# Kernel tuning notes

Hardware: AMD Instinct MI355X
Metric: run time of the kernel (lower is better)

The kernel has to match this reference:

```python
import jax, jax.numpy as jnp
import numpy as np
from jax import lax

# --- config (matches init_kwargs) ---
H = 1024          # hidden_size
I = 704           # moe_intermediate_size (per expert)
E = 32            # n_routed_experts
G = 8             # n_group
TOPK_GROUP = 3    # topk_group
K = 6             # num_experts_per_tok
N_SHARED = 2      # n_shared_experts -> shared intermediate = N_SHARED * I
SCALE = 1.0       # routed_scaling_factor
T = 2048          # number of tokens
CAP = 2 * (T * K) // E


def setup_inputs() -> dict:
    key = jax.random.key(0)
    ks = jax.random.split(key, 8)
    s = 0.02  # initializer_range
    Is = N_SHARED * I
    return {
        "x": jax.random.normal(ks[0], (T, H), jnp.float32),
        "gate_w": s * jax.random.normal(ks[1], (E, H), jnp.float32),   # router
        "w_gate": s * jax.random.normal(ks[2], (E, H, I), jnp.float32),
        "w_up":   s * jax.random.normal(ks[3], (E, H, I), jnp.float32),
        "w_down": s * jax.random.normal(ks[4], (E, I, H), jnp.float32),
        "sw_gate": s * jax.random.normal(ks[5], (H, Is), jnp.float32),
        "sw_up":   s * jax.random.normal(ks[6], (H, Is), jnp.float32),
        "sw_down": s * jax.random.normal(ks[7], (Is, H), jnp.float32),
    }


def _moe_forward(x, gate_w, w_gate, w_up, w_down, sw_gate, sw_up, sw_down):
    # ---- router: softmax scores + group-limited top-k (topk_method='gready') ----
    logits = x @ gate_w.T                                  # [T, E]
    scores = jax.nn.softmax(logits, axis=-1)               # [T, E]
    group_scores = scores.reshape(T, G, E // G).max(-1)    # [T, G]
    _, gidx = lax.top_k(group_scores, TOPK_GROUP)          # [T, topk_group]
    gmask = jnp.zeros((T, G), scores.dtype).at[jnp.arange(T)[:, None], gidx].set(1.0)
    emask = jnp.repeat(gmask, E // G, axis=1)              # [T, E]
    masked_scores = jnp.where(emask > 0, scores, 0.0)
    topk_w, topk_idx = lax.top_k(masked_scores, K)         # [T, K]
    # norm_topk_prob=False -> weights are raw softmax scores * routed_scaling_factor
    topk_w = topk_w * SCALE

    # ---- dispatch: sort assignments by expert, scatter into [E, CAP, H] buffers ----
    flat_e = topk_idx.reshape(-1)                          # [T*K]
    order = jnp.argsort(flat_e)
    se = flat_e[order]                                     # sorted expert ids
    tok = order // K                                       # source token of each slot
    counts = jax.ops.segment_sum(jnp.ones_like(flat_e), flat_e, num_segments=E)
    starts = jnp.cumsum(counts) - counts
    pos = jnp.arange(T * K) - starts[se]                   # position within expert
    valid = pos < CAP
    pos_w = jnp.where(valid, pos, CAP)                     # overflow slot CAP (sliced off)
    xbuf = jnp.zeros((E, CAP + 1, H), x.dtype).at[se, pos_w].set(x[tok])
    xb = xbuf[:, :CAP]                                     # [E, CAP, H]

    # ---- grouped expert MLPs: silu(x Wg) * (x Wu) @ Wd ----
    g = jnp.einsum("ech,ehi->eci", xb, w_gate)
    u = jnp.einsum("ech,ehi->eci", xb, w_up)
    yb = jnp.einsum("eci,eih->ech", jax.nn.silu(g) * u, w_down)  # [E, CAP, H]

    # ---- combine: gather back and weighted-scatter to tokens ----
    y_flat = yb[se, jnp.minimum(pos, CAP - 1)] * valid[:, None].astype(x.dtype)
    wts = topk_w.reshape(-1)[order]                        # [T*K]
    routed = jnp.zeros((T, H), x.dtype).at[tok].add(y_flat * wts[:, None])

    # ---- shared experts MLP (intermediate = n_shared * moe_inter) ----
    sg = jax.nn.silu(x @ sw_gate) * (x @ sw_up)
    shared = sg @ sw_down

    return routed + shared                                 # [T, H]


def reference(x, gate_w, w_gate, w_up, w_down, sw_gate, sw_up, sw_down):
    return _moe_forward(x, gate_w, w_gate, w_up, w_down, sw_gate, sw_up, sw_down)
```

## Files before the change

### kernel.cpp

```cpp
#include <hip/hip_runtime.h>
#include <hip/hip_bf16.h>

#define H 1024
#define I_DIM 704
#define E 32
#define TOPK_GROUP 3
#define K_TOP 6
#define T_TOK 2048
#define CAP 768
#define IS_DIM 1408
#define NCHUNK 192

typedef __attribute__((ext_vector_type(8))) short short8v;
typedef __attribute__((ext_vector_type(4))) float f32x4;

__device__ __forceinline__ unsigned short f2bfbits(float f) {
  unsigned u = __float_as_uint(f);
  unsigned r = (u + 0x7fffu + ((u >> 16) & 1u)) >> 16;
  return (unsigned short)r;
}
__device__ __forceinline__ unsigned packbf2(float lo, float hi) {
  return (unsigned)f2bfbits(lo) | ((unsigned)f2bfbits(hi) << 16);
}
__device__ __forceinline__ void gload_lds16(const short* g, short* l) {
  __builtin_amdgcn_global_load_lds(
      (const __attribute__((address_space(1))) unsigned int*)g,
      (__attribute__((address_space(3))) unsigned int*)l, 16, 0, 0);
}

__global__ void cast_x_kernel(const float* __restrict__ x, short* __restrict__ xb) {
  size_t i = ((size_t)blockIdx.x * 256 + threadIdx.x) * 4;
  float4 v = *(const float4*)(x + i);
  short4 s;
  s.x = (short)f2bfbits(v.x); s.y = (short)f2bfbits(v.y);
  s.z = (short)f2bfbits(v.z); s.w = (short)f2bfbits(v.w);
  *(short4*)(xb + i) = s;
}

__global__ __launch_bounds__(256) void transpose_cast_kernel(
    const float* __restrict__ in, short* __restrict__ outp,
    int C, int N, long long in_stride, long long out_stride) {
  int e = blockIdx.z;
  const float* src = in + (long long)e * in_stride;
  short* dst = outp + (long long)e * out_stride;
  int n0 = blockIdx.x * 64, c0 = blockIdx.y * 64;
  __shared__ unsigned ldsb[64][34];
  int t = threadIdx.x;
  int n4 = t & 15;
  int kp = t >> 4;
  #pragma unroll
  for (int p = 0; p < 2; ++p) {
    int c = c0 + p * 32 + 2 * kp;
    const float* s0 = src + (long long)c * N + n0 + 4 * n4;
    float4 a = *(const float4*)s0;
    float4 b = *(const float4*)(s0 + N);
    int cc = p * 16 + kp;
    ldsb[4 * n4 + 0][cc] = packbf2(a.x, b.x);
    ldsb[4 * n4 + 1][cc] = packbf2(a.y, b.y);
    ldsb[4 * n4 + 2][cc] = packbf2(a.z, b.z);
    ldsb[4 * n4 + 3][cc] = packbf2(a.w, b.w);
  }
  __syncthreads();
  int ch = t & 7;
  int nr = t >> 3;
  #pragma unroll
  for (int p = 0; p < 2; ++p) {
    int n = p * 32 + nr;
    uint4 v;
    v.x = ldsb[n][4 * ch + 0]; v.y = ldsb[n][4 * ch + 1];
    v.z = ldsb[n][4 * ch + 2]; v.w = ldsb[n][4 * ch + 3];
    *(uint4*)(dst + (size_t)(n0 + n) * C + c0 + 8 * ch) = v;
  }
}

__global__ __launch_bounds__(64) void gating_kernel(const float* __restrict__ x,
                                                    const float* __restrict__ gw,
                                                    int* __restrict__ tidx,
                                                    float* __restrict__ tw) {
  int t = blockIdx.x;
  int lane = threadIdx.x;
  int e = lane & 31, half = lane >> 5;
  const float4* xr4 = (const float4*)(x + (size_t)t * H + half * 512);
  const float4* wr4 = (const float4*)(gw + (size_t)e * H + half * 512);
  double acc = 0.0;
  #pragma unroll 4
  for (int j = 0; j < 128; ++j) {
    float4 a = xr4[j], b = wr4[j];
    acc += (double)a.x * b.x + (double)a.y * b.y + (double)a.z * b.z + (double)a.w * b.w;
  }
  acc += __shfl_down(acc, 32);
  double lg = acc;
  double m = lg;
  #pragma unroll
  for (int off = 16; off >= 1; off >>= 1) {
    double o = __shfl_xor(m, off);
    if (o > m) m = o;
  }
  double p = exp(lg - m);
  double sum = p;
  #pragma unroll
  for (int off = 16; off >= 1; off >>= 1) sum += __shfl_xor(sum, off);
  p /= sum;
  double gmax = p;
  { double o = __shfl_xor(gmax, 1); if (o > gmax) gmax = o;
    o = __shfl_xor(gmax, 2); if (o > gmax) gmax = o; }
  bool gsel = false;
  double gv = gmax;
  #pragma unroll
  for (int it = 0; it < TOPK_GROUP; ++it) {
    double v = gv; int gi = e >> 2;
    #pragma unroll
    for (int off = 16; off >= 1; off >>= 1) {
      double ov = __shfl_xor(v, off);
      int oi = __shfl_xor(gi, off);
      if (ov > v || (ov == v && oi < gi)) { v = ov; gi = oi; }
    }
    if ((e >> 2) == gi) { gsel = true; gv = -1e300; }
  }
  double mp = gsel ? p : 0.0;
  #pragma unroll
  for (int it = 0; it < K_TOP; ++it) {
    double v = mp; int ei = e;
    #pragma unroll
    for (int off = 16; off >= 1; off >>= 1) {
      double ov = __shfl_xor(v, off);
      int oi = __shfl_xor(ei, off);
      if (ov > v || (ov == v && oi < ei)) { v = ov; ei = oi; }
    }
    if (lane == 0) { tidx[t * K_TOP + it] = ei; tw[t * K_TOP + it] = (float)v; }
    if (e == ei) mp = -2.0;
  }
}

__global__ __launch_bounds__(64) void hist_kernel(const int* __restrict__ tidx,
                                                  int* __restrict__ chunk_hist) {
  __shared__ int h[E];
  int c = blockIdx.x, lane = threadIdx.x;
  if (lane < E) h[lane] = 0;
  __syncthreads();
  int te = tidx[c * 64 + lane];
  atomicAdd(&h[te], 1);
  __syncthreads();
  if (lane < E) chunk_hist[c * E + lane] = h[lane];
}

__global__ __launch_bounds__(1024) void scan_kernel(const int* __restrict__ chunk_hist,
                                                    int* __restrict__ chunk_base,
                                                    int* __restrict__ cnt) {
  __shared__ int h[NCHUNK * E];
  int t = threadIdx.x;
  for (int i = t; i < NCHUNK * E; i += 1024) h[i] = chunk_hist[i];
  __syncthreads();
  if (t < E) {
    int run = 0;
    for (int c = 0; c < NCHUNK; ++c) {
      int v = h[c * E + t];
      h[c * E + t] = run;
      run += v;
    }
    cnt[t] = run < CAP ? run : CAP;
  }
  __syncthreads();
  for (int i = t; i < NCHUNK * E; i += 1024) chunk_base[i] = h[i];
}

__global__ __launch_bounds__(64) void place_kernel(const int* __restrict__ tidx,
                                                   const float* __restrict__ tw,
                                                   const int* __restrict__ chunk_base,
                                                   int* __restrict__ token_list,
                                                   float* __restrict__ slot_w) {
  int c = blockIdx.x, lane = threadIdx.x;
  int idx = c * 64 + lane;
  int te = tidx[idx];
  unsigned long long mymask = 0;
  #pragma unroll
  for (int e = 0; e < E; ++e) {
    unsigned long long bal = __ballot(te == e);
    if (te == e) mymask = bal;
  }
  int rank = __popcll(mymask & ((1ull << lane) - 1ull));
  int pos = chunk_base[c * E + te] + rank;
  if (pos < CAP) {
    token_list[te * CAP + pos] = idx / K_TOP;
    slot_w[te * CAP + pos] = tw[idx];
  }
}

__global__ __launch_bounds__(256) void gateup_kernel(
    const short* __restrict__ Xb, const short* __restrict__ WgT, const short* __restrict__ WuT,
    short* __restrict__ Sout, const int* __restrict__ tlist, const int* __restrict__ cnt_dev,
    int Nld, long long wstride, long long sstride) {
  int e = blockIdx.z;
  int cnt = cnt_dev ? cnt_dev[e] : T_TOK;
  int row0 = blockIdx.y * 128;
  if (row0 >= cnt) return;
  int col0 = blockIdx.x * 64;
  const short* wg = WgT + (long long)e * wstride;
  const short* wu = WuT + (long long)e * wstride;
  short* sbase = Sout + (long long)e * sstride;

  __shared__ __align__(16) short As[128 * 32];
  __shared__ __align__(16) short Bgs[64 * 32];
  __shared__ __align__(16) short Bus[64 * 32];

  int tid = threadIdx.x;
  int lane = tid & 63, wave = tid >> 6;
  int rr = tid >> 2, ch = tid & 3;

  int ra0 = row0 + rr, ra1 = ra0 + 64;
  if (tlist) {
    const int* tl = tlist + e * CAP;
    ra0 = tl[min(ra0, cnt - 1)];
    ra1 = tl[min(ra1, cnt - 1)];
  }
  const short* pa0 = Xb + (size_t)ra0 * H + ch * 8;
  const short* pa1 = Xb + (size_t)ra1 * H + ch * 8;
  const short* pbg = wg + (size_t)(col0 + rr) * H + ch * 8;
  const short* pbu = wu + (size_t)(col0 + rr) * H + ch * 8;

  short* ldsA0 = &As[(wave * 16) * 32];
  short* ldsA1 = &As[(64 + wave * 16) * 32];
  short* ldsBg = &Bgs[(wave * 16) * 32];
  short* ldsBu = &Bus[(wave * 16) * 32];

  int wm = wave & 1, wn = wave >> 1;
  int c = lane & 15, q = lane >> 4;
  const short* fA = &As[(wm * 64 + c) * 32 + q * 8];
  const short* fBg = &Bgs[(wn * 32 + c) * 32 + q * 8];
  const short* fBu = &Bus[(wn * 32 + c) * 32 + q * 8];

  f32x4 accg[4][2], accu[4][2];
  #pragma unroll
  for (int i = 0; i < 4; ++i)
    #pragma unroll
    for (int j = 0; j < 2; ++j) {
      accg[i][j] = (f32x4){0.f, 0.f, 0.f, 0.f};
      accu[i][j] = (f32x4){0.f, 0.f, 0.f, 0.f};
    }

  for (int k0 = 0; k0 < H; k0 += 32) {
    __syncthreads();
    gload_lds16(pa0 + k0, ldsA0);
    gload_lds16(pa1 + k0, ldsA1);
    gload_lds16(pbg + k0, ldsBg);
    gload_lds16(pbu + k0, ldsBu);
    __syncthreads();
    short8v a[4], bg[2], bu[2];
    #pragma unroll
    for (int mi = 0; mi < 4; ++mi) a[mi] = *(const short8v*)(fA + mi * 16 * 32);
    #pragma unroll
    for (int ni = 0; ni < 2; ++ni) {
      bg[ni] = *(const short8v*)(fBg + ni * 16 * 32);
      bu[ni] = *(const short8v*)(fBu + ni * 16 * 32);
    }
    #pragma unroll
    for (int mi = 0; mi < 4; ++mi)
      #pragma unroll
      for (int ni = 0; ni < 2; ++ni) {
        accg[mi][ni] = __builtin_amdgcn_mfma_f32_16x16x32_bf16(a[mi], bg[ni], accg[mi][ni], 0, 0, 0);
        accu[mi][ni] = __builtin_amdgcn_mfma_f32_16x16x32_bf16(a[mi], bu[ni], accu[mi][ni], 0, 0, 0);
      }
  }
  #pragma unroll
  for (int mi = 0; mi < 4; ++mi) {
    int rbase = row0 + wm * 64 + mi * 16 + q * 4;
    #pragma unroll
    for (int ni = 0; ni < 2; ++ni) {
      int col = col0 + wn * 32 + ni * 16 + c;
      #pragma unroll
      for (int r = 0; r < 4; ++r) {
        float g = accg[mi][ni][r], u = accu[mi][ni][r];
        float s = (g / (1.f + __expf(-g))) * u;
        sbase[(size_t)(rbase + r) * Nld + col] = (short)f2bfbits(s);
      }
    }
  }
}

__global__ __launch_bounds__(256) void down_kernel(
    const short* __restrict__ Sin, const short* __restrict__ WdT, float* __restrict__ out,
    const int* __restrict__ tlist, const float* __restrict__ slot_w, const int* __restrict__ cnt_dev,
    int Kdim, long long wstride, long long sstride) {
  int e = blockIdx.z;
  int cnt = cnt_dev ? cnt_dev[e] : T_TOK;
  int row0 = blockIdx.y * 128;
  if (row0 >= cnt) return;
  int col0 = blockIdx.x * 128;
  const short* sb = Sin + (long long)e * sstride;
  const short* wd = WdT + (long long)e * wstride;

  __shared__ __align__(16) short As[128 * 32];
  __shared__ __align__(16) short Bs[128 * 32];

  int tid = threadIdx.x;
  int lane = tid & 63, wave = tid >> 6;
  int rr = tid >> 2, ch = tid & 3;

  const short* pa0 = sb + (size_t)(row0 + rr) * Kdim + ch * 8;
  const short* pa1 = pa0 + (size_t)64 * Kdim;
  const short* pb0 = wd + (size_t)(col0 + rr) * Kdim + ch * 8;
  const short* pb1 = pb0 + (size_t)64 * Kdim;

  short* ldsA0 = &As[(wave * 16) * 32];
  short* ldsA1 = &As[(64 + wave * 16) * 32];
  short* ldsB0 = &Bs[(wave * 16) * 32];
  short* ldsB1 = &Bs[(64 + wave * 16) * 32];

  int wm = wave & 1, wn = wave >> 1;
  int c = lane & 15, q = lane >> 4;
  const short* fA = &As[(wm * 64 + c) * 32 + q * 8];
  const short* fB = &Bs[(wn * 64 + c) * 32 + q * 8];

  f32x4 acc[4][4];
  #pragma unroll
  for (int i = 0; i < 4; ++i)
    #pragma unroll
    for (int j = 0; j < 4; ++j) acc[i][j] = (f32x4){0.f, 0.f, 0.f, 0.f};

  for (int k0 = 0; k0 < Kdim; k0 += 32) {
    __syncthreads();
    gload_lds16(pa0 + k0, ldsA0);
    gload_lds16(pa1 + k0, ldsA1);
    gload_lds16(pb0 + k0, ldsB0);
    gload_lds16(pb1 + k0, ldsB1);
    __syncthreads();
    short8v a[4], b[4];
    #pragma unroll
    for (int mi = 0; mi < 4; ++mi) a[mi] = *(const short8v*)(fA + mi * 16 * 32);
    #pragma unroll
    for (int ni = 0; ni < 4; ++ni) b[ni] = *(const short8v*)(fB + ni * 16 * 32);
    #pragma unroll
    for (int mi = 0; mi < 4; ++mi)
      #pragma unroll
      for (int ni = 0; ni < 4; ++ni)
        acc[mi][ni] = __builtin_amdgcn_mfma_f32_16x16x32_bf16(a[mi], b[ni], acc[mi][ni], 0, 0, 0);
  }

  if (tlist) {
    const int* tl = tlist + e * CAP;
    const float* swt = slot_w + e * CAP;
    #pragma unroll
    for (int mi = 0; mi < 4; ++mi) {
      int rb = row0 + wm * 64 + mi * 16 + q * 4;
      #pragma unroll
      for (int r = 0; r < 4; ++r) {
        int s = rb + r;
        if (s < cnt) {
          int tkn = tl[s];
          float w = swt[s];
          #pragma unroll
          for (int ni = 0; ni < 4; ++ni) {
            int col = col0 + wn * 64 + ni * 16 + c;
            atomicAdd(&out[(size_t)tkn * H + col], w * acc[mi][ni][r]);
          }
        }
      }
    }
  } else {
    #pragma unroll
    for (int mi = 0; mi < 4; ++mi) {
      int rb = row0 + wm * 64 + mi * 16 + q * 4;
      #pragma unroll
      for (int ni = 0; ni < 4; ++ni) {
        int col = col0 + wn * 64 + ni * 16 + c;
        #pragma unroll
        for (int r = 0; r < 4; ++r)
          out[(size_t)(rb + r) * H + col] = acc[mi][ni][r];
      }
    }
  }
}

extern "C" void kernel_launch(void* const* d_in, const int* in_sizes, int n_in,
                              void* d_out, int out_size, void* d_ws, size_t ws_size,
                              hipStream_t stream) {
  const float* x       = (const float*)d_in[0];
  const float* gate_w  = (const float*)d_in[1];
  const float* w_gate  = (const float*)d_in[2];
  const float* w_up    = (const float*)d_in[3];
  const float* w_down  = (const float*)d_in[4];
  const float* sw_gate = (const float*)d_in[5];
  const float* sw_up   = (const float*)d_in[6];
  const float* sw_down = (const float*)d_in[7];
  float* out = (float*)d_out;
  char* ws = (char*)d_ws;

  size_t o = 0;
  short* xb   = (short*)(ws + o); o += (size_t)T_TOK * H * 2;
  short* Sr   = (short*)(ws + o); o += (size_t)E * CAP * I_DIM * 2;
  short* Ss   = (short*)(ws + o); o += (size_t)T_TOK * IS_DIM * 2;
  short* wgT  = (short*)(ws + o); o += (size_t)E * I_DIM * H * 2;
  short* wuT  = (short*)(ws + o); o += (size_t)E * I_DIM * H * 2;
  short* wdT  = (short*)(ws + o); o += (size_t)E * H * I_DIM * 2;
  short* swgT = (short*)(ws + o); o += (size_t)IS_DIM * H * 2;
  short* swuT = (short*)(ws + o); o += (size_t)IS_DIM * H * 2;
  short* swdT = (short*)(ws + o); o += (size_t)H * IS_DIM * 2;
  int*   tidx = (int*)(ws + o);   o += (size_t)T_TOK * K_TOP * 4;
  float* twt  = (float*)(ws + o); o += (size_t)T_TOK * K_TOP * 4;
  int*   tl   = (int*)(ws + o);   o += (size_t)E * CAP * 4;
  float* swt  = (float*)(ws + o); o += (size_t)E * CAP * 4;
  int*   cnt  = (int*)(ws + o);   o += 256;
  int*   chist = (int*)(ws + o);  o += (size_t)NCHUNK * E * 4;
  int*   cbase = (int*)(ws + o);  o += (size_t)NCHUNK * E * 4;

  cast_x_kernel<<<(T_TOK * H) / 1024, 256, 0, stream>>>(x, xb);
  gating_kernel<<<T_TOK, 64, 0, stream>>>(x, gate_w, tidx, twt);
  hist_kernel<<<NCHUNK, 64, 0, stream>>>(tidx, chist);
  scan_kernel<<<1, 1024, 0, stream>>>(chist, cbase, cnt);
  place_kernel<<<NCHUNK, 64, 0, stream>>>(tidx, twt, cbase, tl, swt);

  transpose_cast_kernel<<<dim3(I_DIM / 64, H / 64, E), 256, 0, stream>>>(
      w_gate, wgT, H, I_DIM, (long long)H * I_DIM, (long long)I_DIM * H);
  transpose_cast_kernel<<<dim3(I_DIM / 64, H / 64, E), 256, 0, stream>>>(
      w_up, wuT, H, I_DIM, (long long)H * I_DIM, (long long)I_DIM * H);
  transpose_cast_kernel<<<dim3(H / 64, I_DIM / 64, E), 256, 0, stream>>>(
      w_down, wdT, I_DIM, H, (long long)I_DIM * H, (long long)H * I_DIM);
  transpose_cast_kernel<<<dim3(IS_DIM / 64, H / 64, 1), 256, 0, stream>>>(
      sw_gate, swgT, H, IS_DIM, 0, 0);
  transpose_cast_kernel<<<dim3(IS_DIM / 64, H / 64, 1), 256, 0, stream>>>(
      sw_up, swuT, H, IS_DIM, 0, 0);
  transpose_cast_kernel<<<dim3(H / 64, IS_DIM / 64, 1), 256, 0, stream>>>(
      sw_down, swdT, IS_DIM, H, 0, 0);

  gateup_kernel<<<dim3(I_DIM / 64, CAP / 128, E), 256, 0, stream>>>(
      xb, wgT, wuT, Sr, tl, cnt, I_DIM, (long long)I_DIM * H, (long long)CAP * I_DIM);
  gateup_kernel<<<dim3(IS_DIM / 64, T_TOK / 128, 1), 256, 0, stream>>>(
      xb, swgT, swuT, Ss, nullptr, nullptr, IS_DIM, 0, 0);
  down_kernel<<<dim3(H / 128, T_TOK / 128, 1), 256, 0, stream>>>(
      Ss, swdT, out, nullptr, nullptr, nullptr, IS_DIM, 0, 0);
  down_kernel<<<dim3(H / 128, CAP / 128, E), 256, 0, stream>>>(
      Sr, wdT, out, tl, swt, cnt, I_DIM, (long long)H * I_DIM, (long long)CAP * I_DIM);
}
```

Before: 564.2 us.

## Fuse weight fp32-to-bf16 cast into GEMM loads and replace atomics with combine kernel

Drops the separate transpose/cast kernels for all expert and shared weights. The GEMM kernels now read fp32 weights directly, convert them to bf16 in registers and write them into LDS in transposed layout. The routed down-projection now writes bf16 per-slot outputs to a buffer instead of doing float atomics. A new combine kernel gathers each token's top-k slot outputs with their weights and adds them to the shared output. This avoids a full read-write pass over the weights and the atomic contention, at the cost of reading twice as many weight bytes inside the GEMMs (fp32 instead of bf16) and an extra Yr write/read round trip.

```diff
diff --git a/kernel.cpp b/kernel.cpp
--- a/kernel.cpp
+++ b/kernel.cpp
@@ -20,7 +20,11 @@
   return (unsigned short)r;
 }
 __device__ __forceinline__ unsigned packbf2(float lo, float hi) {
-  return (unsigned)f2bfbits(lo) | ((unsigned)f2bfbits(hi) << 16);
+  __hip_bfloat162 h = __float22bfloat162_rn(make_float2(lo, hi));
+  unsigned u; __builtin_memcpy(&u, &h, 4); return u;
+}
+__device__ __forceinline__ float bf2f(unsigned short b) {
+  return __uint_as_float(((unsigned)b) << 16);
 }
 __device__ __forceinline__ void gload_lds16(const short* g, short* l) {
   __builtin_amdgcn_global_load_lds(
@@ -35,42 +39,6 @@
   s.x = (short)f2bfbits(v.x); s.y = (short)f2bfbits(v.y);
   s.z = (short)f2bfbits(v.z); s.w = (short)f2bfbits(v.w);
   *(short4*)(xb + i) = s;
-}
-
-__global__ __launch_bounds__(256) void transpose_cast_kernel(
-    const float* __restrict__ in, short* __restrict__ outp,
-    int C, int N, long long in_stride, long long out_stride) {
-  int e = blockIdx.z;
-  const float* src = in + (long long)e * in_stride;
-  short* dst = outp + (long long)e * out_stride;
-  int n0 = blockIdx.x * 64, c0 = blockIdx.y * 64;
-  __shared__ unsigned ldsb[64][34];
-  int t = threadIdx.x;
-  int n4 = t & 15;
-  int kp = t >> 4;
-  #pragma unroll
-  for (int p = 0; p < 2; ++p) {
-    int c = c0 + p * 32 + 2 * kp;
-    const float* s0 = src + (long long)c * N + n0 + 4 * n4;
-    float4 a = *(const float4*)s0;
-    float4 b = *(const float4*)(s0 + N);
-    int cc = p * 16 + kp;
-    ldsb[4 * n4 + 0][cc] = packbf2(a.x, b.x);
-    ldsb[4 * n4 + 1][cc] = packbf2(a.y, b.y);
-    ldsb[4 * n4 + 2][cc] = packbf2(a.z, b.z);
-    ldsb[4 * n4 + 3][cc] = packbf2(a.w, b.w);
-  }
-  __syncthreads();
-  int ch = t & 7;
-  int nr = t >> 3;
-  #pragma unroll
-  for (int p = 0; p < 2; ++p) {
-    int n = p * 32 + nr;
-    uint4 v;
-    v.x = ldsb[n][4 * ch + 0]; v.y = ldsb[n][4 * ch + 1];
-    v.z = ldsb[n][4 * ch + 2]; v.w = ldsb[n][4 * ch + 3];
-    *(uint4*)(dst + (size_t)(n0 + n) * C + c0 + 8 * ch) = v;
-  }
 }
 
 __global__ __launch_bounds__(64) void gating_kernel(const float* __restrict__ x,
@@ -165,10 +133,9 @@
 }
 
 __global__ __launch_bounds__(64) void place_kernel(const int* __restrict__ tidx,
-                                                   const float* __restrict__ tw,
                                                    const int* __restrict__ chunk_base,
                                                    int* __restrict__ token_list,
-                                                   float* __restrict__ slot_w) {
+                                                   int* __restrict__ sid) {
   int c = blockIdx.x, lane = threadIdx.x;
   int idx = c * 64 + lane;
   int te = tidx[idx];
@@ -180,14 +147,16 @@
   }
   int rank = __popcll(mymask & ((1ull << lane) - 1ull));
   int pos = chunk_base[c * E + te] + rank;
+  int s = -1;
   if (pos < CAP) {
     token_list[te * CAP + pos] = idx / K_TOP;
-    slot_w[te * CAP + pos] = tw[idx];
-  }
+    s = te * CAP + pos;
+  }
+  sid[idx] = s;
 }
 
 __global__ __launch_bounds__(256) void gateup_kernel(
-    const short* __restrict__ Xb, const short* __restrict__ WgT, const short* __restrict__ WuT,
+    const short* __restrict__ Xb, const float* __restrict__ Wg, const float* __restrict__ Wu,
     short* __restrict__ Sout, const int* __restrict__ tlist, const int* __restrict__ cnt_dev,
     int Nld, long long wstride, long long sstride) {
   int e = blockIdx.z;
@@ -195,8 +164,8 @@
   int row0 = blockIdx.y * 128;
   if (row0 >= cnt) return;
   int col0 = blockIdx.x * 64;
-  const short* wg = WgT + (long long)e * wstride;
-  const short* wu = WuT + (long long)e * wstride;
+  const float* wg = Wg + (long long)e * wstride;
+  const float* wu = Wu + (long long)e * wstride;
   short* sbase = Sout + (long long)e * sstride;
 
   __shared__ __align__(16) short As[128 * 32];
@@ -205,8 +174,8 @@
 
   int tid = threadIdx.x;
   int lane = tid & 63, wave = tid >> 6;
+
   int rr = tid >> 2, ch = tid & 3;
-
   int ra0 = row0 + rr, ra1 = ra0 + 64;
   if (tlist) {
     const int* tl = tlist + e * CAP;
@@ -215,13 +184,14 @@
   }
   const short* pa0 = Xb + (size_t)ra0 * H + ch * 8;
   const short* pa1 = Xb + (size_t)ra1 * H + ch * 8;
-  const short* pbg = wg + (size_t)(col0 + rr) * H + ch * 8;
-  const short* pbu = wu + (size_t)(col0 + rr) * H + ch * 8;
-
   short* ldsA0 = &As[(wave * 16) * 32];
   short* ldsA1 = &As[(64 + wave * 16) * 32];
-  short* ldsBg = &Bgs[(wave * 16) * 32];
-  short* ldsBu = &Bus[(wave * 16) * 32];
+
+  int bn = lane, kb = wave * 8;
+  const float* pg = wg + (size_t)kb * Nld + col0 + bn;
+  const float* pu = wu + (size_t)kb * Nld + col0 + bn;
+  short* ldsBg = &Bgs[bn * 32 + kb];
+  short* ldsBu = &Bus[bn * 32 + kb];
 
   int wm = wave & 1, wn = wave >> 1;
   int c = lane & 15, q = lane >> 4;
@@ -239,11 +209,24 @@
     }
 
   for (int k0 = 0; k0 < H; k0 += 32) {
+    float gv[8], uv[8];
+    const float* pgk = pg + (size_t)k0 * Nld;
+    const float* puk = pu + (size_t)k0 * Nld;
+    #pragma unroll
+    for (int j = 0; j < 8; ++j) {
+      gv[j] = pgk[(size_t)j * Nld];
+      uv[j] = puk[(size_t)j * Nld];
+    }
     __syncthreads();
     gload_lds16(pa0 + k0, ldsA0);
     gload_lds16(pa1 + k0, ldsA1);
-    gload_lds16(pbg + k0, ldsBg);
-    gload_lds16(pbu + k0, ldsBu);
+    uint4 wvg, wvu;
+    wvg.x = packbf2(gv[0], gv[1]); wvg.y = packbf2(gv[2], gv[3]);
+    wvg.z = packbf2(gv[4], gv[5]); wvg.w = packbf2(gv[6], gv[7]);
+    wvu.x = packbf2(uv[0], uv[1]); wvu.y = packbf2(uv[2], uv[3]);
+    wvu.z = packbf2(uv[4], uv[5]); wvu.w = packbf2(uv[6], uv[7]);
+    *(uint4*)ldsBg = wvg;
+    *(uint4*)ldsBu = wvu;
     __syncthreads();
     short8v a[4], bg[2], bu[2];
     #pragma unroll
@@ -278,16 +261,16 @@
 }
 
 __global__ __launch_bounds__(256) void down_kernel(
-    const short* __restrict__ Sin, const short* __restrict__ WdT, float* __restrict__ out,
-    const int* __restrict__ tlist, const float* __restrict__ slot_w, const int* __restrict__ cnt_dev,
-    int Kdim, long long wstride, long long sstride) {
+    const short* __restrict__ Sin, const float* __restrict__ Wd,
+    float* __restrict__ outF, short* __restrict__ outY,
+    const int* __restrict__ cnt_dev, int Kdim, long long wstride, long long sstride) {
   int e = blockIdx.z;
   int cnt = cnt_dev ? cnt_dev[e] : T_TOK;
   int row0 = blockIdx.y * 128;
   if (row0 >= cnt) return;
   int col0 = blockIdx.x * 128;
   const short* sb = Sin + (long long)e * sstride;
-  const short* wd = WdT + (long long)e * wstride;
+  const float* wd = Wd + (long long)e * wstride;
 
   __shared__ __align__(16) short As[128 * 32];
   __shared__ __align__(16) short Bs[128 * 32];
@@ -298,13 +281,12 @@
 
   const short* pa0 = sb + (size_t)(row0 + rr) * Kdim + ch * 8;
   const short* pa1 = pa0 + (size_t)64 * Kdim;
-  const short* pb0 = wd + (size_t)(col0 + rr) * Kdim + ch * 8;
-  const short* pb1 = pb0 + (size_t)64 * Kdim;
-
   short* ldsA0 = &As[(wave * 16) * 32];
   short* ldsA1 = &As[(64 + wave * 16) * 32];
-  short* ldsB0 = &Bs[(wave * 16) * 32];
-  short* ldsB1 = &Bs[(64 + wave * 16) * 32];
+
+  int bn = tid & 127, kb = (tid >> 7) * 16;
+  const float* pb = wd + (size_t)kb * H + col0 + bn;
+  short* ldsB = &Bs[bn * 32 + kb];
 
   int wm = wave & 1, wn = wave >> 1;
   int c = lane & 15, q = lane >> 4;
@@ -318,11 +300,20 @@
     for (int j = 0; j < 4; ++j) acc[i][j] = (f32x4){0.f, 0.f, 0.f, 0.f};
 
   for (int k0 = 0; k0 < Kdim; k0 += 32) {
+    float bv[16];
+    const float* pbk = pb + (size_t)k0 * H;
+    #pragma unroll
+    for (int j = 0; j < 16; ++j) bv[j] = pbk[(size_t)j * H];
     __syncthreads();
     gload_lds16(pa0 + k0, ldsA0);
     gload_lds16(pa1 + k0, ldsA1);
-    gload_lds16(pb0 + k0, ldsB0);
-    gload_lds16(pb1 + k0, ldsB1);
+    uint4 w0, w1;
+    w0.x = packbf2(bv[0], bv[1]);  w0.y = packbf2(bv[2], bv[3]);
+    w0.z = packbf2(bv[4], bv[5]);  w0.w = packbf2(bv[6], bv[7]);
+    w1.x = packbf2(bv[8], bv[9]);  w1.y = packbf2(bv[10], bv[11]);
+    w1.z = packbf2(bv[12], bv[13]); w1.w = packbf2(bv[14], bv[15]);
+    *(uint4*)ldsB = w0;
+    *(uint4*)(ldsB + 8) = w1;
     __syncthreads();
     short8v a[4], b[4];
     #pragma unroll
@@ -336,23 +327,17 @@
         acc[mi][ni] = __builtin_amdgcn_mfma_f32_16x16x32_bf16(a[mi], b[ni], acc[mi][ni], 0, 0, 0);
   }
 
-  if (tlist) {
-    const int* tl = tlist + e * CAP;
-    const float* swt = slot_w + e * CAP;
+  if (outY) {
     #pragma unroll
     for (int mi = 0; mi < 4; ++mi) {
       int rb = row0 + wm * 64 + mi * 16 + q * 4;
       #pragma unroll
       for (int r = 0; r < 4; ++r) {
-        int s = rb + r;
-        if (s < cnt) {
-          int tkn = tl[s];
-          float w = swt[s];
-          #pragma unroll
-          for (int ni = 0; ni < 4; ++ni) {
-            int col = col0 + wn * 64 + ni * 16 + c;
-            atomicAdd(&out[(size_t)tkn * H + col], w * acc[mi][ni][r]);
-          }
+        short* yrow = outY + (size_t)(e * CAP + rb + r) * H;
+        #pragma unroll
+        for (int ni = 0; ni < 4; ++ni) {
+          int col = col0 + wn * 64 + ni * 16 + c;
+          yrow[col] = (short)f2bfbits(acc[mi][ni][r]);
         }
       }
     }
@@ -365,10 +350,32 @@
         int col = col0 + wn * 64 + ni * 16 + c;
         #pragma unroll
         for (int r = 0; r < 4; ++r)
-          out[(size_t)(rb + r) * H + col] = acc[mi][ni][r];
+          outF[(size_t)(rb + r) * H + col] = acc[mi][ni][r];
       }
     }
   }
+}
+
+__global__ __launch_bounds__(256) void combine_kernel(
+    const short* __restrict__ Yr, const int* __restrict__ sid,
+    const float* __restrict__ twt, float* __restrict__ out) {
+  int t = blockIdx.x;
+  int col = threadIdx.x * 4;
+  float* op = out + (size_t)t * H + col;
+  float4 o = *(float4*)op;
+  #pragma unroll
+  for (int k = 0; k < K_TOP; ++k) {
+    int s = sid[t * K_TOP + k];
+    if (s >= 0) {
+      float w = twt[t * K_TOP + k];
+      ushort4 y = *(const ushort4*)(Yr + (size_t)s * H + col);
+      o.x += w * bf2f(y.x);
+      o.y += w * bf2f(y.y);
+      o.z += w * bf2f(y.z);
+      o.w += w * bf2f(y.w);
+    }
+  }
+  *(float4*)op = o;
 }
 
 extern "C" void kernel_launch(void* const* d_in, const int* in_sizes, int n_in,
@@ -389,16 +396,11 @@
   short* xb   = (short*)(ws + o); o += (size_t)T_TOK * H * 2;
   short* Sr   = (short*)(ws + o); o += (size_t)E * CAP * I_DIM * 2;
   short* Ss   = (short*)(ws + o); o += (size_t)T_TOK * IS_DIM * 2;
-  short* wgT  = (short*)(ws + o); o += (size_t)E * I_DIM * H * 2;
-  short* wuT  = (short*)(ws + o); o += (size_t)E * I_DIM * H * 2;
-  short* wdT  = (short*)(ws + o); o += (size_t)E * H * I_DIM * 2;
-  short* swgT = (short*)(ws + o); o += (size_t)IS_DIM * H * 2;
-  short* swuT = (short*)(ws + o); o += (size_t)IS_DIM * H * 2;
-  short* swdT = (short*)(ws + o); o += (size_t)H * IS_DIM * 2;
+  short* Yr   = (short*)(ws + o); o += (size_t)E * CAP * H * 2;
   int*   tidx = (int*)(ws + o);   o += (size_t)T_TOK * K_TOP * 4;
   float* twt  = (float*)(ws + o); o += (size_t)T_TOK * K_TOP * 4;
+  int*   sid  = (int*)(ws + o);   o += (size_t)T_TOK * K_TOP * 4;
   int*   tl   = (int*)(ws + o);   o += (size_t)E * CAP * 4;
-  float* swt  = (float*)(ws + o); o += (size_t)E * CAP * 4;
   int*   cnt  = (int*)(ws + o);   o += 256;
   int*   chist = (int*)(ws + o);  o += (size_t)NCHUNK * E * 4;
   int*   cbase = (int*)(ws + o);  o += (size_t)NCHUNK * E * 4;
@@ -407,27 +409,15 @@
   gating_kernel<<<T_TOK, 64, 0, stream>>>(x, gate_w, tidx, twt);
   hist_kernel<<<NCHUNK, 64, 0, stream>>>(tidx, chist);
   scan_kernel<<<1, 1024, 0, stream>>>(chist, cbase, cnt);
-  place_kernel<<<NCHUNK, 64, 0, stream>>>(tidx, twt, cbase, tl, swt);
-
-  transpose_cast_kernel<<<dim3(I_DIM / 64, H / 64, E), 256, 0, stream>>>(
-      w_gate, wgT, H, I_DIM, (long long)H * I_DIM, (long long)I_DIM * H);
-  transpose_cast_kernel<<<dim3(I_DIM / 64, H / 64, E), 256, 0, stream>>>(
-      w_up, wuT, H, I_DIM, (long long)H * I_DIM, (long long)I_DIM * H);
-  transpose_cast_kernel<<<dim3(H / 64, I_DIM / 64, E), 256, 0, stream>>>(
-      w_down, wdT, I_DIM, H, (long long)I_DIM * H, (long long)H * I_DIM);
-  transpose_cast_kernel<<<dim3(IS_DIM / 64, H / 64, 1), 256, 0, stream>>>(
-      sw_gate, swgT, H, IS_DIM, 0, 0);
-  transpose_cast_kernel<<<dim3(IS_DIM / 64, H / 64, 1), 256, 0, stream>>>(
-      sw_up, swuT, H, IS_DIM, 0, 0);
-  transpose_cast_kernel<<<dim3(H / 64, IS_DIM / 64, 1), 256, 0, stream>>>(
-      sw_down, swdT, IS_DIM, H, 0, 0);
+  place_kernel<<<NCHUNK, 64, 0, stream>>>(tidx, cbase, tl, sid);
 
   gateup_kernel<<<dim3(I_DIM / 64, CAP / 128, E), 256, 0, stream>>>(
-      xb, wgT, wuT, Sr, tl, cnt, I_DIM, (long long)I_DIM * H, (long long)CAP * I_DIM);
+      xb, w_gate, w_up, Sr, tl, cnt, I_DIM, (long long)H * I_DIM, (long long)CAP * I_DIM);
   gateup_kernel<<<dim3(IS_DIM / 64, T_TOK / 128, 1), 256, 0, stream>>>(
-      xb, swgT, swuT, Ss, nullptr, nullptr, IS_DIM, 0, 0);
+      xb, sw_gate, sw_up, Ss, nullptr, nullptr, IS_DIM, 0, 0);
   down_kernel<<<dim3(H / 128, T_TOK / 128, 1), 256, 0, stream>>>(
-      Ss, swdT, out, nullptr, nullptr, nullptr, IS_DIM, 0, 0);
+      Ss, sw_down, out, nullptr, nullptr, IS_DIM, 0, 0);
   down_kernel<<<dim3(H / 128, CAP / 128, E), 256, 0, stream>>>(
-      Sr, wdT, out, tl, swt, cnt, I_DIM, (long long)H * I_DIM, (long long)CAP * I_DIM);
-}
+      Sr, w_down, nullptr, Yr, cnt, I_DIM, (long long)I_DIM * H, (long long)CAP * I_DIM);
+  combine_kernel<<<T_TOK, 256, 0, stream>>>(Yr, sid, twt, out);
+}
```

After: 552.7 us. 1.02x faster.
